# Performance work log

Hardware: AMD Instinct MI355X
Metric: run time of the kernel (lower is better)

The kernel has to match this reference:

```python
import jax, jax.numpy as jnp
import numpy as np

L = 4          # decoder layers (model_config "[4,[0],0]")
D = 1024       # d_model
H = 16         # n_head
DH = 64        # d_head
DI = 4096      # d_inner
V = 16000      # n_token (add_eot=False)
S = 1024       # seq len
B = 4          # batch
EPS = 1e-5


def _layer_norm(x, g, b):
    mu = jnp.mean(x, axis=-1, keepdims=True)
    var = jnp.mean(jnp.square(x - mu), axis=-1, keepdims=True)
    return (x - mu) * jax.lax.rsqrt(var + EPS) * g + b


def _rel_shift(x):
    # x: [b, n, q, k]
    b, n, q, k = x.shape
    zero_pad = jnp.zeros((b, n, q, 1), dtype=x.dtype)
    xp = jnp.concatenate([zero_pad, x], axis=3)        # [b,n,q,k+1]
    xp = xp.reshape(b, n, k + 1, q)
    return xp[:, :, 1:, :].reshape(b, n, q, k)


def setup_inputs() -> dict:
    key = jax.random.key(0)
    ks = list(jax.random.split(key, 24))
    sd = 0.02
    inp = {}
    inp["tokens"] = jax.random.randint(ks[0], (S, B), 0, V)
    inp["word_emb"] = jax.random.normal(ks[1], (V, D), jnp.float32) * sd
    inp["r_w_bias"] = jax.random.normal(ks[2], (H, DH), jnp.float32) * sd
    inp["r_r_bias"] = jax.random.normal(ks[3], (H, DH), jnp.float32) * sd
    inp["qkv_w"] = jax.random.normal(ks[4], (L, D, 3 * H * DH), jnp.float32) * sd
    inp["qkv_b"] = jnp.zeros((L, 3 * H * DH), jnp.float32)
    inp["r_kw"] = jax.random.normal(ks[5], (L, D, H * DH), jnp.float32) * sd
    inp["r_kb"] = jnp.zeros((L, H * DH), jnp.float32)
    inp["o_w"] = jax.random.normal(ks[6], (L, H * DH, D), jnp.float32) * sd
    inp["o_b"] = jnp.zeros((L, D), jnp.float32)
    inp["ln1_g"] = jnp.ones((L, D), jnp.float32)
    inp["ln1_b"] = jnp.zeros((L, D), jnp.float32)
    inp["ff1_w"] = jax.random.normal(ks[7], (L, D, DI), jnp.float32) * sd
    inp["ff1_b"] = jnp.zeros((L, DI), jnp.float32)
    inp["ff2_w"] = jax.random.normal(ks[8], (L, DI, D), jnp.float32) * sd
    inp["ff2_b"] = jnp.zeros((L, D), jnp.float32)
    inp["ln2_g"] = jnp.ones((L, D), jnp.float32)
    inp["ln2_b"] = jnp.zeros((L, D), jnp.float32)
    inp["final_w"] = jax.random.normal(ks[9], (D, V), jnp.float32) * sd
    inp["final_b"] = jnp.zeros((V,), jnp.float32)
    return inp


def reference(tokens, word_emb, r_w_bias, r_r_bias, qkv_w, qkv_b, r_kw, r_kb,
              o_w, o_b, ln1_g, ln1_b, ff1_w, ff1_b, ff2_w, ff2_b,
              ln2_g, ln2_b, final_w, final_b):
    s, b = tokens.shape
    h = word_emb[tokens]                                 # [S,B,D]
    # sinusoidal relative positions, pos_seq = klen-1 ... 0
    pos_seq = jnp.arange(s - 1, -1, -1, dtype=h.dtype)
    inv_freq = 1.0 / (10000.0 ** (jnp.arange(0, D, 2, dtype=h.dtype) / D))
    sinu = pos_seq[:, None] * inv_freq[None, :]
    r = jnp.concatenate([jnp.sin(sinu), jnp.cos(sinu)], axis=-1)   # [S,D]
    # causal mask: True = masked (j > i)
    mask = jnp.triu(jnp.ones((s, s), dtype=bool), k=1)
    scale = 1.0 / (DH ** 0.5)
    neg_inf = jnp.asarray(-jnp.inf, dtype=h.dtype)

    for l in range(L):
        qkv = h @ qkv_w[l] + qkv_b[l]                    # [S,B,3*H*DH]
        q, k, v = jnp.split(qkv, 3, axis=-1)
        q = q.reshape(s, b, H, DH)
        k = k.reshape(s, b, H, DH)
        v = v.reshape(s, b, H, DH)
        rk = (r @ r_kw[l] + r_kb[l]).reshape(s, H, DH)   # [S,H,DH]
        AC = jnp.einsum('ibnd,jbnd->bnij', q + r_w_bias, k)
        BD = jnp.einsum('ibnd,jnd->bnij', q + r_r_bias, rk)
        BD = _rel_shift(BD)
        score = scale * (AC + BD)
        score = jnp.where(mask[None, None, :, :], neg_inf, score)
        prob = jax.nn.softmax(score, axis=-1)
        vec = jnp.einsum('bnij,jbnd->ibnd', prob, v).reshape(s, b, H * DH)
        attn_out = vec @ o_w[l] + o_b[l]
        h = _layer_norm(h + attn_out, ln1_g[l], ln1_b[l])
        ff = jax.nn.gelu(h @ ff1_w[l] + ff1_b[l], approximate=False) @ ff2_w[l] + ff2_b[l]
        h = _layer_norm(h + ff, ln2_g[l], ln2_b[l])

    logits = h @ final_w + final_b                       # [S,B,V]
    return logits
```

## Files before the change

### kernel.cpp

```cpp
#include <hip/hip_runtime.h>

#define S 1024
#define Bb 4
#define Hh 16
#define DHh 64
#define Dm 1024
#define DIi 4096
#define Vv 16000
#define Lll 4

typedef __attribute__((ext_vector_type(4))) float f32x4;
typedef __attribute__((ext_vector_type(8))) __bf16 bf16x8;
typedef __attribute__((ext_vector_type(8))) unsigned short u16x8;
typedef __attribute__((ext_vector_type(4))) unsigned short u16x4;

__device__ __forceinline__ unsigned short f2bf(float f) {
  unsigned int u = __float_as_uint(f);
  u += 0x7fffu + ((u >> 16) & 1u);
  return (unsigned short)(u >> 16);
}
__device__ __forceinline__ float bf2f(unsigned short u) {
  return __uint_as_float(((unsigned int)u) << 16);
}

__device__ __forceinline__ void gload_lds16(const void* g, void* l) {
  __builtin_amdgcn_global_load_lds((const __attribute__((address_space(1))) unsigned int*)g,
                                   (__attribute__((address_space(3))) unsigned int*)l, 16, 0, 0);
}

__device__ __forceinline__ f32x4 mfma_bf16(bf16x8 a, bf16x8 b, f32x4 c) {
  return __builtin_amdgcn_mfma_f32_16x16x32_bf16(a, b, c, 0, 0, 0);
}

__global__ __launch_bounds__(256) void embed_k(const int* __restrict__ tokens,
                                               const float* __restrict__ we,
                                               float* __restrict__ h,
                                               unsigned short* __restrict__ hb) {
  int row = blockIdx.x;
  int t = threadIdx.x;
  int tok = tokens[row];
  f32x4 v = *(const f32x4*)&we[(long)tok * Dm + t * 4];
  *(f32x4*)&h[(long)row * Dm + t * 4] = v;
  u16x4 r;
#pragma unroll
  for (int e = 0; e < 4; ++e) r[e] = f2bf(v[e]);
  *(u16x4*)&hb[(long)row * Dm + t * 4] = r;
}

__global__ __launch_bounds__(256) void posr_k(unsigned short* __restrict__ r) {
  int idx = blockIdx.x * 256 + threadIdx.x;
  int u = idx >> 10, d = idx & 1023;
  float pos = (float)(S - 1 - u);
  int j = d & 511;
  float invf = powf(10000.0f, -(float)j * (1.0f / 512.0f));
  float a = pos * invf;
  r[idx] = f2bf(d < 512 ? sinf(a) : cosf(a));
}

__global__ __launch_bounds__(256) void wcvt_t(const float* __restrict__ W,
                                              unsigned short* __restrict__ WT,
                                              int Kd, int Nd) {
  __shared__ unsigned short tile[32][40];
  int n0 = blockIdx.x * 32, k0 = blockIdx.y * 32;
  const float* Wb = W + (long)blockIdx.z * Kd * Nd;
  unsigned short* WTb = WT + (long)blockIdx.z * Kd * Nd;
  int t = threadIdx.x;
  int rr = t >> 3, c4 = (t & 7) * 4;
  f32x4 v = *(const f32x4*)&Wb[(long)(k0 + rr) * Nd + n0 + c4];
#pragma unroll
  for (int e = 0; e < 4; ++e) tile[rr][c4 + e] = f2bf(v[e]);
  __syncthreads();
  if (t < 128) {
    int n = t >> 2, k8 = (t & 3) * 8;
    u16x8 pk;
#pragma unroll
    for (int e = 0; e < 8; ++e) pk[e] = tile[k8 + e][n];
    *(u16x8*)&WTb[(long)(n0 + n) * Kd + k0 + k8] = pk;
  }
}

template <int EPI>
__global__ __launch_bounds__(256) void gemm_bt(const unsigned short* __restrict__ A,
                                               const unsigned short* __restrict__ BT,
                                               const float* __restrict__ bias,
                                               void* __restrict__ Cout,
                                               int M, int N, int K, int ntn) {
  __shared__ unsigned short As[128 * 64];
  __shared__ unsigned short Bs[128 * 64];
  const int tid = threadIdx.x;
  const int lane = tid & 63;
  const int w = tid >> 6;
  const int nwg = gridDim.x;
  const int qq = nwg >> 3, rr = nwg & 7;
  const int xcd = blockIdx.x & 7, loc = blockIdx.x >> 3;
  const int wg = (xcd < rr ? xcd * (qq + 1) : rr * (qq + 1) + (xcd - rr) * qq) + loc;
  const int bn = (wg % ntn) * 128, bm = (wg / ntn) * 128;
  const int wr = (w >> 1) * 64, wc = (w & 1) * 64;
  const int la = lane & 15, lk = (lane >> 4) * 8;
  f32x4 acc[4][4] = {};

  const int rrow = tid >> 3;
  const int rcol = (tid & 7) * 8;
  const unsigned short* ag = A + (long)(bm + rrow) * K + rcol;
  const unsigned short* bg = BT + (long)(bn + rrow) * K + rcol;

  for (int k0 = 0; k0 < K; k0 += 64) {
    __syncthreads();
#pragma unroll
    for (int c = 0; c < 4; ++c) {
      gload_lds16(ag + (long)c * 32 * K + k0, &As[c * 2048 + w * 512]);
      gload_lds16(bg + (long)c * 32 * K + k0, &Bs[c * 2048 + w * 512]);
    }
    __syncthreads();
#pragma unroll
    for (int kk = 0; kk < 2; ++kk) {
      bf16x8 af[4], bq[4];
#pragma unroll
      for (int mi = 0; mi < 4; ++mi)
        af[mi] = *(const bf16x8*)&As[(wr + mi * 16 + la) * 64 + kk * 32 + lk];
#pragma unroll
      for (int ni = 0; ni < 4; ++ni)
        bq[ni] = *(const bf16x8*)&Bs[(wc + ni * 16 + la) * 64 + kk * 32 + lk];
#pragma unroll
      for (int mi = 0; mi < 4; ++mi)
#pragma unroll
        for (int ni = 0; ni < 4; ++ni)
          acc[mi][ni] = mfma_bf16(af[mi], bq[ni], acc[mi][ni]);
    }
  }
  const int cr = (lane >> 4) * 4;
#pragma unroll
  for (int mi = 0; mi < 4; ++mi) {
#pragma unroll
    for (int ni = 0; ni < 4; ++ni) {
      int col = bn + wc + ni * 16 + la;
      float bv = bias[col];
      int row = bm + wr + mi * 16 + cr;
#pragma unroll
      for (int e = 0; e < 4; ++e) {
        float v = acc[mi][ni][e] + bv;
        if (EPI == 0) {
          ((float*)Cout)[(long)(row + e) * N + col] = v;
        } else if (EPI == 1) {
          ((unsigned short*)Cout)[(long)(row + e) * N + col] = f2bf(v);
        } else {
          float g = 0.5f * v * (1.0f + erff(v * 0.70710678118f));
          ((unsigned short*)Cout)[(long)(row + e) * N + col] = f2bf(g);
        }
      }
    }
  }
}

__global__ __launch_bounds__(256) void qkv_prep(const unsigned short* __restrict__ q3,
                                                const float* __restrict__ rwb,
                                                const float* __restrict__ rrb,
                                                unsigned short* __restrict__ qw,
                                                unsigned short* __restrict__ qr,
                                                unsigned short* __restrict__ kb) {
  int idx = blockIdx.x * 256 + threadIdx.x;
  int c8 = (idx & 127) * 8;
  int row = idx >> 7;
  int s = row >> 2, b = row & 3;
  int n = c8 >> 6, d = c8 & 63;
  u16x8 qv = *(const u16x8*)&q3[(long)row * 3072 + c8];
  u16x8 kv = *(const u16x8*)&q3[(long)row * 3072 + 1024 + c8];
  long o = ((long)(b * Hh + n) * S + s) * 64 + d;
  u16x8 ow, orr;
#pragma unroll
  for (int e = 0; e < 8; ++e) {
    float q = bf2f(qv[e]);
    ow[e] = f2bf(q + rwb[c8 + e]);
    orr[e] = f2bf(q + rrb[c8 + e]);
  }
  *(u16x8*)&qw[o] = ow;
  *(u16x8*)&qr[o] = orr;
  *(u16x8*)&kb[o] = kv;
}

__global__ __launch_bounds__(256) void vt_prep(const unsigned short* __restrict__ q3,
                                               unsigned short* __restrict__ vT) {
  __shared__ unsigned short tile[64][72];
  const int it = blockIdx.x, bn = blockIdx.y;
  const int nh = bn & 15, bbv = bn >> 4;
  const int t = threadIdx.x;
  const int i0 = t >> 3, c8 = (t & 7) * 8;
#pragma unroll
  for (int c = 0; c < 2; ++c) {
    int i = i0 + c * 32;
    u16x8 v = *(const u16x8*)&q3[((long)(it * 64 + i) * Bb + bbv) * 3072 + 2048 + nh * 64 + c8];
    *(u16x8*)&tile[i][c8] = v;
  }
  __syncthreads();
  for (int cc = t; cc < 512; cc += 256) {
    int d = cc >> 3, i8 = (cc & 7) * 8;
    u16x8 pk;
#pragma unroll
    for (int e = 0; e < 8; ++e) pk[e] = tile[i8 + e][d];
    *(u16x8*)&vT[((long)bn * 64 + d) * S + it * 64 + i8] = pk;
  }
}

__global__ __launch_bounds__(256) void rkb_prep(const unsigned short* __restrict__ rkall,
                                                unsigned short* __restrict__ rkb) {
  int idx = blockIdx.x * 256 + threadIdx.x;
  int d8 = (idx & 7) * 8;
  int u = (idx >> 3) & 1023;
  int nl = idx >> 13;
  int l = nl >> 4, n = nl & 15;
  u16x8 v = *(const u16x8*)&rkall[(long)u * 4096 + l * 1024 + n * 64 + d8];
  *(u16x8*)&rkb[(long)idx * 8] = v;
}

__global__ __launch_bounds__(256) void attn_k(const unsigned short* __restrict__ qw,
                                              const unsigned short* __restrict__ qr,
                                              const unsigned short* __restrict__ kbuf,
                                              const unsigned short* __restrict__ vT,
                                              const unsigned short* __restrict__ rk,
                                              unsigned short* __restrict__ vec) {
  __shared__ unsigned short Ks[2][64 * 64];
  __shared__ unsigned short Vs[2][64 * 64];
  __shared__ unsigned short plds[4][16][72];
  const int tid = threadIdx.x, lane = tid & 63, w = tid >> 6;
  const int bn = blockIdx.x >> 3, pr = blockIdx.x & 7;
  const int nh = bn & 15, bbv = bn >> 4;
  const int la = lane & 15, hi = lane >> 4, lk = hi * 8;
  const int hi4 = hi * 4;
  const unsigned short* kbase = kbuf + (long)bn * S * 64;
  const unsigned short* vbase = vT + (long)bn * 64 * S;
  const unsigned short* rbase = rk + (long)nh * S * 64;

  const int q0 = w * 128 + lane;
  const int r0 = q0 >> 3, c0s = (q0 & 7) ^ (r0 & 7);
  const int q1 = q0 + 64;
  const int r1 = q1 >> 3, c1s = (q1 & 7) ^ (r1 & 7);

  int cur = 0;
#pragma unroll 1
  for (int half = 0; half < 2; ++half) {
    const int it = half ? (15 - pr) : pr;
    const int iw = it * 64 + w * 16;
    bf16x8 qwf[2], qrf[2];
    {
      const unsigned short* qp = qw + ((long)bn * S + iw + la) * 64 + lk;
      qwf[0] = *(const bf16x8*)qp;
      qwf[1] = *(const bf16x8*)(qp + 32);
      const unsigned short* qp2 = qr + ((long)bn * S + iw + la) * 64 + lk;
      qrf[0] = *(const bf16x8*)qp2;
      qrf[1] = *(const bf16x8*)(qp2 + 32);
    }
    f32x4 opv[4] = {};
    float m_[4] = {-3e38f, -3e38f, -3e38f, -3e38f};
    float l_[4] = {0.f, 0.f, 0.f, 0.f};

    gload_lds16(kbase + (long)r0 * 64 + c0s * 8, &Ks[cur][w * 1024]);
    gload_lds16(kbase + (long)r1 * 64 + c1s * 8, &Ks[cur][w * 1024 + 512]);
    gload_lds16(vbase + (long)r0 * S + c0s * 8, &Vs[cur][w * 1024]);
    gload_lds16(vbase + (long)r1 * S + c1s * 8, &Vs[cur][w * 1024 + 512]);
    __syncthreads();

    for (int jt = 0; jt <= it; ++jt) {
      const int j0 = jt * 64;
      const bool edge = (jt == it);
      if (jt < it) {
        const int jn = j0 + 64;
        gload_lds16(kbase + (long)(jn + r0) * 64 + c0s * 8, &Ks[cur ^ 1][w * 1024]);
        gload_lds16(kbase + (long)(jn + r1) * 64 + c1s * 8, &Ks[cur ^ 1][w * 1024 + 512]);
        gload_lds16(vbase + (long)r0 * S + jn + c0s * 8, &Vs[cur ^ 1][w * 1024]);
        gload_lds16(vbase + (long)r1 * S + jn + c1s * 8, &Vs[cur ^ 1][w * 1024 + 512]);
      }
      const int u0 = S - 16 - iw + j0;
      bf16x8 rf[10];
#pragma unroll
      for (int g = 0; g < 5; ++g) {
        int u = u0 + g * 16 + la;
        if (edge) u = (u > S - 1) ? (S - 1) : u;
        const unsigned short* rp = rbase + (long)u * 64 + lk;
        rf[2 * g] = *(const bf16x8*)rp;
        rf[2 * g + 1] = *(const bf16x8*)(rp + 32);
      }
      f32x4 ac[4] = {};
#pragma unroll
      for (int f = 0; f < 4; ++f) {
        int row = f * 16 + la;
        const unsigned short* kl = &Ks[cur][row * 64];
        bf16x8 k0 = *(const bf16x8*)(kl + (((hi) ^ (row & 7)) << 3));
        bf16x8 k1 = *(const bf16x8*)(kl + (((hi + 4) ^ (row & 7)) << 3));
        ac[f] = mfma_bf16(qwf[0], k0, ac[f]);
        ac[f] = mfma_bf16(qwf[1], k1, ac[f]);
      }
      f32x4 gg[5] = {};
#pragma unroll
      for (int g = 0; g < 5; ++g) {
        gg[g] = mfma_bf16(qrf[0], rf[2 * g], gg[g]);
        gg[g] = mfma_bf16(qrf[1], rf[2 * g + 1], gg[g]);
      }
      float p[4][4];
#pragma unroll
      for (int f = 0; f < 4; ++f) {
#pragma unroll
        for (int e = 0; e < 4; ++e) {
          int r = hi4 + e;
          float x = (la >= 15 - r) ? gg[f][e] : gg[f + 1][e];
          int src = (lane & 48) | ((la + 15 - r) & 15);
          float bd = __shfl(x, src, 64);
          float sc = (ac[f][e] + bd) * 0.125f;
          if (edge) {
            int i_ = iw + r, j_ = j0 + f * 16 + la;
            sc = (j_ > i_) ? -1e30f : sc;
          }
          p[f][e] = sc;
        }
      }
#pragma unroll
      for (int e = 0; e < 4; ++e) {
        float mx = fmaxf(fmaxf(p[0][e], p[1][e]), fmaxf(p[2][e], p[3][e]));
#pragma unroll
        for (int o = 1; o < 16; o <<= 1) mx = fmaxf(mx, __shfl_xor(mx, o, 64));
        float mnew = fmaxf(m_[e], mx);
        float alpha = __expf(m_[e] - mnew);
        m_[e] = mnew;
        float rs = 0.f;
#pragma unroll
        for (int f = 0; f < 4; ++f) {
          p[f][e] = __expf(p[f][e] - mnew);
          rs += p[f][e];
        }
        l_[e] = l_[e] * alpha + rs;
#pragma unroll
        for (int d = 0; d < 4; ++d) opv[d][e] *= alpha;
      }
#pragma unroll
      for (int f = 0; f < 4; ++f)
#pragma unroll
        for (int e = 0; e < 4; ++e)
          plds[w][hi4 + e][f * 16 + la] = f2bf(p[f][e]);
      bf16x8 pa0 = *(const bf16x8*)&plds[w][la][lk];
      bf16x8 pa1 = *(const bf16x8*)&plds[w][la][32 + lk];
#pragma unroll
      for (int d = 0; d < 4; ++d) {
        int dd = d * 16 + la;
        const unsigned short* vl = &Vs[cur][dd * 64];
        bf16x8 v0 = *(const bf16x8*)(vl + (((hi) ^ (dd & 7)) << 3));
        bf16x8 v1 = *(const bf16x8*)(vl + (((hi + 4) ^ (dd & 7)) << 3));
        opv[d] = mfma_bf16(pa0, v0, opv[d]);
        opv[d] = mfma_bf16(pa1, v1, opv[d]);
      }
      __syncthreads();
      if (jt < it) cur ^= 1;
    }
#pragma unroll
    for (int e = 0; e < 4; ++e) {
#pragma unroll
      for (int o = 1; o < 16; o <<= 1) l_[e] += __shfl_xor(l_[e], o, 64);
    }
#pragma unroll
    for (int d = 0; d < 4; ++d) {
#pragma unroll
      for (int e = 0; e < 4; ++e) {
        int i_ = iw + hi4 + e;
        int col = nh * 64 + d * 16 + la;
        vec[((long)i_ * Bb + bbv) * 1024 + col] = f2bf(opv[d][e] / l_[e]);
      }
    }
  }
}

__global__ __launch_bounds__(256) void add_ln(float* __restrict__ h, const float* __restrict__ x,
                                              const float* __restrict__ g, const float* __restrict__ b,
                                              unsigned short* __restrict__ hb) {
  __shared__ float red[8];
  int row = blockIdx.x, t = threadIdx.x;
  long base = (long)row * 1024 + t * 4;
  f32x4 hv = *(const f32x4*)&h[base];
  f32x4 xv = *(const f32x4*)&x[base];
  f32x4 y = hv + xv;
  float s = y[0] + y[1] + y[2] + y[3];
  float q = y[0] * y[0] + y[1] * y[1] + y[2] * y[2] + y[3] * y[3];
#pragma unroll
  for (int o = 1; o < 64; o <<= 1) {
    s += __shfl_xor(s, o, 64);
    q += __shfl_xor(q, o, 64);
  }
  int w = t >> 6, lane = t & 63;
  if (lane == 0) { red[w] = s; red[4 + w] = q; }
  __syncthreads();
  s = red[0] + red[1] + red[2] + red[3];
  q = red[4] + red[5] + red[6] + red[7];
  float mu = s * (1.0f / 1024.0f);
  float var = q * (1.0f / 1024.0f) - mu * mu;
  float rstd = rsqrtf(var + 1e-5f);
  f32x4 gv = *(const f32x4*)&g[t * 4];
  f32x4 bv = *(const f32x4*)&b[t * 4];
  f32x4 o;
  u16x4 ob;
#pragma unroll
  for (int e = 0; e < 4; ++e) {
    o[e] = (y[e] - mu) * rstd * gv[e] + bv[e];
    ob[e] = f2bf(o[e]);
  }
  *(f32x4*)&h[base] = o;
  *(u16x4*)&hb[base] = ob;
}

extern "C" void kernel_launch(void* const* d_in, const int* in_sizes, int n_in,
                              void* d_out, int out_size, void* d_ws, size_t ws_size,
                              hipStream_t stream) {
  const int* tokens = (const int*)d_in[0];
  const float* word_emb = (const float*)d_in[1];
  const float* rwb = (const float*)d_in[2];
  const float* rrb = (const float*)d_in[3];
  const float* qkv_w = (const float*)d_in[4];
  const float* qkv_b = (const float*)d_in[5];
  const float* r_kw = (const float*)d_in[6];
  const float* r_kb = (const float*)d_in[7];
  const float* o_w = (const float*)d_in[8];
  const float* o_b = (const float*)d_in[9];
  const float* ln1g = (const float*)d_in[10];
  const float* ln1b = (const float*)d_in[11];
  const float* ff1w = (const float*)d_in[12];
  const float* ff1b = (const float*)d_in[13];
  const float* ff2w = (const float*)d_in[14];
  const float* ff2b = (const float*)d_in[15];
  const float* ln2g = (const float*)d_in[16];
  const float* ln2b = (const float*)d_in[17];
  const float* fw = (const float*)d_in[18];
  const float* fb = (const float*)d_in[19];

  char* ws = (char*)d_ws;
  unsigned short* WBF = (unsigned short*)(ws);
  float* H = (float*)(ws + 33554432);
  unsigned short* HB = (unsigned short*)(ws + 50331648);
  unsigned short* GB = (unsigned short*)(ws + 58720256);
  unsigned short* RBF = (unsigned short*)(ws + 92274688);

  char* ob = (char*)d_out;
  float* OUTF = (float*)ob;
  unsigned short* OUTH = (unsigned short*)ob;
  unsigned short* QW = (unsigned short*)(ob + 67108864);
  unsigned short* QR = (unsigned short*)(ob + 75497472);
  unsigned short* KB = (unsigned short*)(ob + 83886080);
  unsigned short* VT = (unsigned short*)(ob + 92274688);
  unsigned short* RKB = (unsigned short*)(ob + 100663296);
  float* OUT = (float*)d_out;

  embed_k<<<4096, 256, 0, stream>>>(tokens, word_emb, H, HB);
  posr_k<<<4096, 256, 0, stream>>>(RBF);
  wcvt_t<<<dim3(32, 32, 4), 256, 0, stream>>>(r_kw, WBF, 1024, 1024);
  gemm_bt<1><<<256, 256, 0, stream>>>(RBF, WBF, r_kb, OUTH, 1024, 4096, 1024, 32);
  rkb_prep<<<2048, 256, 0, stream>>>(OUTH, RKB);

  for (int l = 0; l < Lll; ++l) {
    wcvt_t<<<dim3(96, 32, 1), 256, 0, stream>>>(qkv_w + (long)l * 1024 * 3072, WBF, 1024, 3072);
    gemm_bt<1><<<768, 256, 0, stream>>>(HB, WBF, qkv_b + l * 3072, OUTH, 4096, 3072, 1024, 24);
    qkv_prep<<<2048, 256, 0, stream>>>(OUTH, rwb, rrb, QW, QR, KB);
    vt_prep<<<dim3(16, 64), 256, 0, stream>>>(OUTH, VT);
    attn_k<<<512, 256, 0, stream>>>(QW, QR, KB, VT, RKB + (long)l * Hh * S * 64, HB);
    wcvt_t<<<dim3(32, 32, 1), 256, 0, stream>>>(o_w + (long)l * 1024 * 1024, WBF, 1024, 1024);
    gemm_bt<0><<<256, 256, 0, stream>>>(HB, WBF, o_b + l * 1024, OUTF, 4096, 1024, 1024, 8);
    add_ln<<<4096, 256, 0, stream>>>(H, OUTF, ln1g + l * 1024, ln1b + l * 1024, HB);

    wcvt_t<<<dim3(128, 32, 1), 256, 0, stream>>>(ff1w + (long)l * 1024 * 4096, WBF, 1024, 4096);
    gemm_bt<2><<<1024, 256, 0, stream>>>(HB, WBF, ff1b + l * 4096, GB, 4096, 4096, 1024, 32);
    wcvt_t<<<dim3(32, 128, 1), 256, 0, stream>>>(ff2w + (long)l * 4096 * 1024, WBF, 4096, 1024);
    gemm_bt<0><<<256, 256, 0, stream>>>(GB, WBF, ff2b + l * 1024, OUTF, 4096, 1024, 4096, 8);
    add_ln<<<4096, 256, 0, stream>>>(H, OUTF, ln2g + l * 1024, ln2b + l * 1024, HB);
  }

  wcvt_t<<<dim3(500, 32, 1), 256, 0, stream>>>(fw, WBF, 1024, 16000);
  gemm_bt<0><<<4000, 256, 0, stream>>>(HB, WBF, fb, OUT, 4096, 16000, 1024, 125);
}
```

Measured before the change: 1.700 ms.

## Replace 128x128 GEMM with 256x256 tiled, 4-stage pipelined GEMM kernel

Replaces the single-buffered 128x128 bf16 GEMM with a 512-thread 256x256 tile kernel. It uses a 4-deep LDS ring of K=32 slices loaded asynchronously, explicit vmcnt waits with one barrier per step, and raised priority around the MFMA block. The larger tile raises arithmetic intensity and the pipeline overlaps global loads with compute. The final projection pads N to 16128 with bounds checks, and weight conversion zero-fills out-of-range columns. The risks are small grids for the N=1024 GEMMs (only 64 workgroups, underfilling the GPU's many CUs) and higher register and LDS pressure.

```diff
diff --git a/kernel.cpp b/kernel.cpp
--- a/kernel.cpp
+++ b/kernel.cpp
@@ -62,11 +62,13 @@
                                               int Kd, int Nd) {
   __shared__ unsigned short tile[32][40];
   int n0 = blockIdx.x * 32, k0 = blockIdx.y * 32;
+  const bool inb = n0 < Nd;
   const float* Wb = W + (long)blockIdx.z * Kd * Nd;
   unsigned short* WTb = WT + (long)blockIdx.z * Kd * Nd;
   int t = threadIdx.x;
   int rr = t >> 3, c4 = (t & 7) * 4;
-  f32x4 v = *(const f32x4*)&Wb[(long)(k0 + rr) * Nd + n0 + c4];
+  f32x4 v = {0.f, 0.f, 0.f, 0.f};
+  if (inb) v = *(const f32x4*)&Wb[(long)(k0 + rr) * Nd + n0 + c4];
 #pragma unroll
   for (int e = 0; e < 4; ++e) tile[rr][c4 + e] = f2bf(v[e]);
   __syncthreads();
@@ -80,72 +82,99 @@
 }
 
 template <int EPI>
-__global__ __launch_bounds__(256) void gemm_bt(const unsigned short* __restrict__ A,
-                                               const unsigned short* __restrict__ BT,
-                                               const float* __restrict__ bias,
-                                               void* __restrict__ Cout,
-                                               int M, int N, int K, int ntn) {
-  __shared__ unsigned short As[128 * 64];
-  __shared__ unsigned short Bs[128 * 64];
-  const int tid = threadIdx.x;
-  const int lane = tid & 63;
-  const int w = tid >> 6;
+__global__ __launch_bounds__(512, 2) void gemm256(const unsigned short* __restrict__ A,
+                                                  const unsigned short* __restrict__ BT,
+                                                  const float* __restrict__ bias,
+                                                  void* __restrict__ Cout,
+                                                  int M, int N, int K,
+                                                  int ntm, int ntn, int morder) {
+  __shared__ unsigned short lds[65536];
+  unsigned short* Al = lds;
+  unsigned short* Bl = lds + 32768;
+  const int tid = threadIdx.x, lane = tid & 63, w = tid >> 6;
+  const int la = lane & 15, hi = lane >> 4;
   const int nwg = gridDim.x;
   const int qq = nwg >> 3, rr = nwg & 7;
   const int xcd = blockIdx.x & 7, loc = blockIdx.x >> 3;
   const int wg = (xcd < rr ? xcd * (qq + 1) : rr * (qq + 1) + (xcd - rr) * qq) + loc;
-  const int bn = (wg % ntn) * 128, bm = (wg / ntn) * 128;
-  const int wr = (w >> 1) * 64, wc = (w & 1) * 64;
-  const int la = lane & 15, lk = (lane >> 4) * 8;
-  f32x4 acc[4][4] = {};
-
-  const int rrow = tid >> 3;
-  const int rcol = (tid & 7) * 8;
-  const unsigned short* ag = A + (long)(bm + rrow) * K + rcol;
-  const unsigned short* bg = BT + (long)(bn + rrow) * K + rcol;
-
-  for (int k0 = 0; k0 < K; k0 += 64) {
-    __syncthreads();
-#pragma unroll
-    for (int c = 0; c < 4; ++c) {
-      gload_lds16(ag + (long)c * 32 * K + k0, &As[c * 2048 + w * 512]);
-      gload_lds16(bg + (long)c * 32 * K + k0, &Bs[c * 2048 + w * 512]);
-    }
-    __syncthreads();
-#pragma unroll
-    for (int kk = 0; kk < 2; ++kk) {
-      bf16x8 af[4], bq[4];
-#pragma unroll
-      for (int mi = 0; mi < 4; ++mi)
-        af[mi] = *(const bf16x8*)&As[(wr + mi * 16 + la) * 64 + kk * 32 + lk];
-#pragma unroll
-      for (int ni = 0; ni < 4; ++ni)
-        bq[ni] = *(const bf16x8*)&Bs[(wc + ni * 16 + la) * 64 + kk * 32 + lk];
-#pragma unroll
-      for (int mi = 0; mi < 4; ++mi)
-#pragma unroll
-        for (int ni = 0; ni < 4; ++ni)
-          acc[mi][ni] = mfma_bf16(af[mi], bq[ni], acc[mi][ni]);
-    }
-  }
-  const int cr = (lane >> 4) * 4;
-#pragma unroll
-  for (int mi = 0; mi < 4; ++mi) {
-#pragma unroll
-    for (int ni = 0; ni < 4; ++ni) {
-      int col = bn + wc + ni * 16 + la;
-      float bv = bias[col];
-      int row = bm + wr + mi * 16 + cr;
-#pragma unroll
-      for (int e = 0; e < 4; ++e) {
-        float v = acc[mi][ni][e] + bv;
-        if (EPI == 0) {
-          ((float*)Cout)[(long)(row + e) * N + col] = v;
-        } else if (EPI == 1) {
-          ((unsigned short*)Cout)[(long)(row + e) * N + col] = f2bf(v);
-        } else {
-          float g = 0.5f * v * (1.0f + erff(v * 0.70710678118f));
-          ((unsigned short*)Cout)[(long)(row + e) * N + col] = f2bf(g);
+  int bm, bn;
+  if (morder) { bm = (wg % ntm) * 256; bn = (wg / ntm) * 256; }
+  else        { bn = (wg % ntn) * 256; bm = (wg / ntn) * 256; }
+  const int wr = w >> 2, wc = w & 3;
+  f32x4 acc[8][4] = {};
+
+  const unsigned short* ag = A + (long)(bm + w * 16 + la) * K + hi * 8;
+  const unsigned short* bg = BT + (long)(bn + w * 16 + la) * K + hi * 8;
+  unsigned short* Asg = Al + w * 512;
+  unsigned short* Bsg = Bl + w * 512;
+  const unsigned short* Ard = Al + wr * 4096 + lane * 8;
+  const unsigned short* Brd = Bl + wc * 2048 + lane * 8;
+  const int NT = K >> 5;
+
+#define STAGE(t) { \
+    long ko_ = (long)(t) * 32; int bo_ = ((t) & 3) * 8192; \
+    gload_lds16(ag + ko_, Asg + bo_); \
+    gload_lds16(ag + ko_ + (long)128 * K, Asg + bo_ + 4096); \
+    gload_lds16(bg + ko_, Bsg + bo_); \
+    gload_lds16(bg + ko_ + (long)128 * K, Bsg + bo_ + 4096); }
+
+#define COMPUTE(t) { \
+    const int bo_ = ((t) & 3) * 8192; \
+    bf16x8 af[8], bq[4]; \
+    _Pragma("unroll") \
+    for (int m = 0; m < 8; ++m) af[m] = *(const bf16x8*)(Ard + bo_ + m * 512); \
+    _Pragma("unroll") \
+    for (int n = 0; n < 4; ++n) bq[n] = *(const bf16x8*)(Brd + bo_ + n * 512); \
+    __builtin_amdgcn_s_setprio(1); \
+    _Pragma("unroll") \
+    for (int m = 0; m < 8; ++m) \
+      _Pragma("unroll") \
+      for (int n = 0; n < 4; ++n) acc[m][n] = mfma_bf16(af[m], bq[n], acc[m][n]); \
+    __builtin_amdgcn_s_setprio(0); }
+
+  STAGE(0); STAGE(1); STAGE(2);
+  int t = 0;
+  for (; t < NT - 3; ++t) {
+    asm volatile("s_waitcnt vmcnt(8)" ::: "memory");
+    __builtin_amdgcn_s_barrier();
+    __builtin_amdgcn_sched_barrier(0);
+    STAGE(t + 3);
+    COMPUTE(t);
+  }
+  asm volatile("s_waitcnt vmcnt(8)" ::: "memory");
+  __builtin_amdgcn_s_barrier();
+  __builtin_amdgcn_sched_barrier(0);
+  COMPUTE(t); ++t;
+  asm volatile("s_waitcnt vmcnt(4)" ::: "memory");
+  __builtin_amdgcn_s_barrier();
+  __builtin_amdgcn_sched_barrier(0);
+  COMPUTE(t); ++t;
+  asm volatile("s_waitcnt vmcnt(0)" ::: "memory");
+  __builtin_amdgcn_s_barrier();
+  __builtin_amdgcn_sched_barrier(0);
+  COMPUTE(t);
+#undef STAGE
+#undef COMPUTE
+
+#pragma unroll
+  for (int m = 0; m < 8; ++m) {
+#pragma unroll
+    for (int n = 0; n < 4; ++n) {
+      int col = bn + wc * 64 + n * 16 + la;
+      if (col < N) {
+        float bv = bias[col];
+        int row = bm + wr * 128 + m * 16 + hi * 4;
+#pragma unroll
+        for (int e = 0; e < 4; ++e) {
+          float v = acc[m][n][e] + bv;
+          if (EPI == 0) {
+            ((float*)Cout)[(long)(row + e) * N + col] = v;
+          } else if (EPI == 1) {
+            ((unsigned short*)Cout)[(long)(row + e) * N + col] = f2bf(v);
+          } else {
+            float g = 0.5f * v * (1.0f + erff(v * 0.70710678118f));
+            ((unsigned short*)Cout)[(long)(row + e) * N + col] = f2bf(g);
+          }
         }
       }
     }
@@ -447,26 +476,26 @@
   embed_k<<<4096, 256, 0, stream>>>(tokens, word_emb, H, HB);
   posr_k<<<4096, 256, 0, stream>>>(RBF);
   wcvt_t<<<dim3(32, 32, 4), 256, 0, stream>>>(r_kw, WBF, 1024, 1024);
-  gemm_bt<1><<<256, 256, 0, stream>>>(RBF, WBF, r_kb, OUTH, 1024, 4096, 1024, 32);
+  gemm256<1><<<64, 512, 0, stream>>>(RBF, WBF, r_kb, OUTH, 1024, 4096, 1024, 4, 16, 0);
   rkb_prep<<<2048, 256, 0, stream>>>(OUTH, RKB);
 
   for (int l = 0; l < Lll; ++l) {
     wcvt_t<<<dim3(96, 32, 1), 256, 0, stream>>>(qkv_w + (long)l * 1024 * 3072, WBF, 1024, 3072);
-    gemm_bt<1><<<768, 256, 0, stream>>>(HB, WBF, qkv_b + l * 3072, OUTH, 4096, 3072, 1024, 24);
+    gemm256<1><<<192, 512, 0, stream>>>(HB, WBF, qkv_b + l * 3072, OUTH, 4096, 3072, 1024, 16, 12, 0);
     qkv_prep<<<2048, 256, 0, stream>>>(OUTH, rwb, rrb, QW, QR, KB);
     vt_prep<<<dim3(16, 64), 256, 0, stream>>>(OUTH, VT);
     attn_k<<<512, 256, 0, stream>>>(QW, QR, KB, VT, RKB + (long)l * Hh * S * 64, HB);
     wcvt_t<<<dim3(32, 32, 1), 256, 0, stream>>>(o_w + (long)l * 1024 * 1024, WBF, 1024, 1024);
-    gemm_bt<0><<<256, 256, 0, stream>>>(HB, WBF, o_b + l * 1024, OUTF, 4096, 1024, 1024, 8);
+    gemm256<0><<<64, 512, 0, stream>>>(HB, WBF, o_b + l * 1024, OUTF, 4096, 1024, 1024, 16, 4, 0);
     add_ln<<<4096, 256, 0, stream>>>(H, OUTF, ln1g + l * 1024, ln1b + l * 1024, HB);
 
     wcvt_t<<<dim3(128, 32, 1), 256, 0, stream>>>(ff1w + (long)l * 1024 * 4096, WBF, 1024, 4096);
-    gemm_bt<2><<<1024, 256, 0, stream>>>(HB, WBF, ff1b + l * 4096, GB, 4096, 4096, 1024, 32);
+    gemm256<2><<<256, 512, 0, stream>>>(HB, WBF, ff1b + l * 4096, GB, 4096, 4096, 1024, 16, 16, 0);
     wcvt_t<<<dim3(32, 128, 1), 256, 0, stream>>>(ff2w + (long)l * 4096 * 1024, WBF, 4096, 1024);
-    gemm_bt<0><<<256, 256, 0, stream>>>(GB, WBF, ff2b + l * 1024, OUTF, 4096, 1024, 4096, 8);
+    gemm256<0><<<64, 512, 0, stream>>>(GB, WBF, ff2b + l * 1024, OUTF, 4096, 1024, 4096, 16, 4, 0);
     add_ln<<<4096, 256, 0, stream>>>(H, OUTF, ln2g + l * 1024, ln2b + l * 1024, HB);
   }
 
-  wcvt_t<<<dim3(500, 32, 1), 256, 0, stream>>>(fw, WBF, 1024, 16000);
-  gemm_bt<0><<<4000, 256, 0, stream>>>(HB, WBF, fb, OUT, 4096, 16000, 1024, 125);
-}
+  wcvt_t<<<dim3(504, 32, 1), 256, 0, stream>>>(fw, WBF, 1024, 16000);
+  gemm256<0><<<1008, 512, 0, stream>>>(HB, WBF, fb, OUT, 4096, 16000, 1024, 16, 63, 1);
+}
```

Result: slower. 2.076 ms (+22.1%).

## Add 256x256 eight-wave GEMM kernel and lazy softmax rescaling in attention

Applied to the files above, without the earlier changes.

Adds a new 512-thread GEMM kernel with 256x256 output tiles, double-buffered direct-to-LDS loads, split fragment loads interleaved with MFMA phases and priority hints. It is used for the QKV, FF1 and final-logits projections. Padding the weight transpose to a multiple of 256 columns lets the last tile handle the ragged vocabulary. Separately, the attention online softmax now tracks one running max per row group and only rescales when the max grows by more than a threshold, which skips exp and multiply work. The lazy rescale risks overflow if values drift, and the larger tiles raise register and LDS pressure.

```diff
diff --git a/kernel.cpp b/kernel.cpp
--- a/kernel.cpp
+++ b/kernel.cpp
@@ -62,11 +62,13 @@
                                               int Kd, int Nd) {
   __shared__ unsigned short tile[32][40];
   int n0 = blockIdx.x * 32, k0 = blockIdx.y * 32;
+  const bool inb = n0 < Nd;
   const float* Wb = W + (long)blockIdx.z * Kd * Nd;
   unsigned short* WTb = WT + (long)blockIdx.z * Kd * Nd;
   int t = threadIdx.x;
   int rr = t >> 3, c4 = (t & 7) * 4;
-  f32x4 v = *(const f32x4*)&Wb[(long)(k0 + rr) * Nd + n0 + c4];
+  f32x4 v = {0.f, 0.f, 0.f, 0.f};
+  if (inb) v = *(const f32x4*)&Wb[(long)(k0 + rr) * Nd + n0 + c4];
 #pragma unroll
   for (int e = 0; e < 4; ++e) tile[rr][c4 + e] = f2bf(v[e]);
   __syncthreads();
@@ -76,6 +78,146 @@
 #pragma unroll
     for (int e = 0; e < 8; ++e) pk[e] = tile[k8 + e][n];
     *(u16x8*)&WTb[(long)(n0 + n) * Kd + k0 + k8] = pk;
+  }
+}
+
+template <int EPI>
+__global__ __launch_bounds__(512, 2) void gemm8(
+    const unsigned short* __restrict__ A, const unsigned short* __restrict__ BT,
+    const float* __restrict__ bias, void* __restrict__ Cout,
+    int M, int N, int K, int ntm, int ntn, int morder) {
+  __shared__ unsigned short lds[65536];
+  const int tid = threadIdx.x, lane = tid & 63, w = tid >> 6;
+  const int la = lane & 15, hi = lane >> 4;
+  const int nwg = gridDim.x;
+  const int qq = nwg >> 3, rr = nwg & 7;
+  const int xcd = blockIdx.x & 7, loc = blockIdx.x >> 3;
+  const int wg = (xcd < rr ? xcd * (qq + 1) : rr * (qq + 1) + (xcd - rr) * qq) + loc;
+  int bm, bn;
+  if (morder) { bm = (wg % ntm) * 256; bn = (wg / ntm) * 256; }
+  else        { bn = (wg % ntn) * 256; bm = (wg / ntn) * 256; }
+  const int wr = w >> 2, wc = w & 3;
+  f32x4 acc[8][4] = {};
+
+  const unsigned short* agS = A + (long)(bm + (w >> 1) * 16 + la) * K + ((w & 1) * 4 + hi) * 8;
+  const unsigned short* bgS = BT + (long)(bn + (w >> 1) * 16 + la) * K + ((w & 1) * 4 + hi) * 8;
+  const long cstep = (long)64 * K;
+  const int aoff = wr * 8192 + hi * 128 + la * 8;
+  const int boff = 32768 + wc * 4096 + hi * 128 + la * 8;
+  const int NT = K >> 6;
+  bf16x8 A0[4][2], A1[4][2], B0[2][2], B1[2][2];
+
+#define STAGE8(tt) { \
+    long ko_ = (long)(tt) * 64; int ab_ = ((tt) & 1) * 16384; \
+    _Pragma("unroll") \
+    for (int c = 0; c < 4; ++c) { \
+      gload_lds16(agS + ko_ + c * cstep, &lds[ab_ + c * 4096 + w * 512]); \
+      gload_lds16(bgS + ko_ + c * cstep, &lds[32768 + ab_ + c * 4096 + w * 512]); } }
+
+#define SYNC_LGKM  __builtin_amdgcn_s_barrier(); \
+    asm volatile("s_waitcnt lgkmcnt(0)" ::: "memory"); \
+    __builtin_amdgcn_sched_barrier(0)
+
+  STAGE8(0); STAGE8(1);
+  asm volatile("s_waitcnt vmcnt(8)" ::: "memory");
+  __builtin_amdgcn_s_barrier();
+
+#pragma unroll 1
+  for (int t = 0; t < NT; ++t) {
+    const int ab = (t & 1) * 16384;
+    const unsigned short* aRd = lds + ab + aoff;
+    const unsigned short* bRd = lds + ab + boff;
+#pragma unroll
+    for (int m = 0; m < 4; ++m)
+#pragma unroll
+      for (int kk = 0; kk < 2; ++kk) A0[m][kk] = *(const bf16x8*)(aRd + m * 1024 + kk * 512);
+#pragma unroll
+    for (int n = 0; n < 2; ++n)
+#pragma unroll
+      for (int kk = 0; kk < 2; ++kk) B0[n][kk] = *(const bf16x8*)(bRd + n * 1024 + kk * 512);
+    SYNC_LGKM;
+    __builtin_amdgcn_s_setprio(1);
+#pragma unroll
+    for (int m = 0; m < 4; ++m)
+#pragma unroll
+      for (int n = 0; n < 2; ++n) {
+        acc[m][n] = mfma_bf16(A0[m][0], B0[n][0], acc[m][n]);
+        acc[m][n] = mfma_bf16(A0[m][1], B0[n][1], acc[m][n]);
+      }
+    __builtin_amdgcn_s_setprio(0);
+    __builtin_amdgcn_s_barrier();
+#pragma unroll
+    for (int n = 0; n < 2; ++n)
+#pragma unroll
+      for (int kk = 0; kk < 2; ++kk) B1[n][kk] = *(const bf16x8*)(bRd + (2 + n) * 1024 + kk * 512);
+    SYNC_LGKM;
+    __builtin_amdgcn_s_setprio(1);
+#pragma unroll
+    for (int m = 0; m < 4; ++m)
+#pragma unroll
+      for (int n = 0; n < 2; ++n) {
+        acc[m][2 + n] = mfma_bf16(A0[m][0], B1[n][0], acc[m][2 + n]);
+        acc[m][2 + n] = mfma_bf16(A0[m][1], B1[n][1], acc[m][2 + n]);
+      }
+    __builtin_amdgcn_s_setprio(0);
+    __builtin_amdgcn_s_barrier();
+#pragma unroll
+    for (int m = 0; m < 4; ++m)
+#pragma unroll
+      for (int kk = 0; kk < 2; ++kk) A1[m][kk] = *(const bf16x8*)(aRd + (4 + m) * 1024 + kk * 512);
+    SYNC_LGKM;
+    __builtin_amdgcn_s_setprio(1);
+#pragma unroll
+    for (int m = 0; m < 4; ++m)
+#pragma unroll
+      for (int n = 0; n < 2; ++n) {
+        acc[4 + m][n] = mfma_bf16(A1[m][0], B0[n][0], acc[4 + m][n]);
+        acc[4 + m][n] = mfma_bf16(A1[m][1], B0[n][1], acc[4 + m][n]);
+      }
+    __builtin_amdgcn_s_setprio(0);
+    __builtin_amdgcn_s_barrier();
+    if (t + 2 < NT) { STAGE8(t + 2); }
+    __builtin_amdgcn_s_setprio(1);
+#pragma unroll
+    for (int m = 0; m < 4; ++m)
+#pragma unroll
+      for (int n = 0; n < 2; ++n) {
+        acc[4 + m][2 + n] = mfma_bf16(A1[m][0], B1[n][0], acc[4 + m][2 + n]);
+        acc[4 + m][2 + n] = mfma_bf16(A1[m][1], B1[n][1], acc[4 + m][2 + n]);
+      }
+    __builtin_amdgcn_s_setprio(0);
+    if (t + 2 < NT) {
+      asm volatile("s_waitcnt vmcnt(8)" ::: "memory");
+    } else if (t + 1 < NT) {
+      asm volatile("s_waitcnt vmcnt(0)" ::: "memory");
+    }
+    __builtin_amdgcn_s_barrier();
+  }
+#undef STAGE8
+#undef SYNC_LGKM
+
+#pragma unroll
+  for (int m = 0; m < 8; ++m) {
+#pragma unroll
+    for (int n = 0; n < 4; ++n) {
+      int col = bn + wc * 64 + n * 16 + la;
+      if (col < N) {
+        float bv = bias[col];
+        int row = bm + wr * 128 + m * 16 + hi * 4;
+#pragma unroll
+        for (int e = 0; e < 4; ++e) {
+          float v = acc[m][n][e] + bv;
+          if (EPI == 0) {
+            ((float*)Cout)[(long)(row + e) * N + col] = v;
+          } else if (EPI == 1) {
+            ((unsigned short*)Cout)[(long)(row + e) * N + col] = f2bf(v);
+          } else {
+            float g = 0.5f * v * (1.0f + erff(v * 0.70710678118f));
+            ((unsigned short*)Cout)[(long)(row + e) * N + col] = f2bf(g);
+          }
+        }
+      }
+    }
   }
 }
 
@@ -250,7 +392,7 @@
       qrf[1] = *(const bf16x8*)(qp2 + 32);
     }
     f32x4 opv[4] = {};
-    float m_[4] = {-3e38f, -3e38f, -3e38f, -3e38f};
+    float m_ = -3e38f;
     float l_[4] = {0.f, 0.f, 0.f, 0.f};
 
     gload_lds16(kbase + (long)r0 * 64 + c0s * 8, &Ks[cur][w * 1024]);
@@ -312,23 +454,33 @@
           p[f][e] = sc;
         }
       }
+      float mx = p[0][0];
+#pragma unroll
+      for (int f = 0; f < 4; ++f)
+#pragma unroll
+        for (int e = 0; e < 4; ++e) mx = fmaxf(mx, p[f][e]);
+#pragma unroll
+      for (int o = 1; o < 16; o <<= 1) mx = fmaxf(mx, __shfl_xor(mx, o, 64));
+      if (!__all(mx <= m_ + 8.0f)) {
+        float mnew = fmaxf(m_, mx);
+        float alpha = __expf(m_ - mnew);
+        m_ = mnew;
+#pragma unroll
+        for (int e = 0; e < 4; ++e) l_[e] *= alpha;
+#pragma unroll
+        for (int d = 0; d < 4; ++d)
+#pragma unroll
+          for (int e = 0; e < 4; ++e) opv[d][e] *= alpha;
+      }
 #pragma unroll
       for (int e = 0; e < 4; ++e) {
-        float mx = fmaxf(fmaxf(p[0][e], p[1][e]), fmaxf(p[2][e], p[3][e]));
-#pragma unroll
-        for (int o = 1; o < 16; o <<= 1) mx = fmaxf(mx, __shfl_xor(mx, o, 64));
-        float mnew = fmaxf(m_[e], mx);
-        float alpha = __expf(m_[e] - mnew);
-        m_[e] = mnew;
         float rs = 0.f;
 #pragma unroll
         for (int f = 0; f < 4; ++f) {
-          p[f][e] = __expf(p[f][e] - mnew);
+          p[f][e] = __expf(p[f][e] - m_);
           rs += p[f][e];
         }
-        l_[e] = l_[e] * alpha + rs;
-#pragma unroll
-        for (int d = 0; d < 4; ++d) opv[d][e] *= alpha;
+        l_[e] += rs;
       }
 #pragma unroll
       for (int f = 0; f < 4; ++f)
@@ -452,7 +604,7 @@
 
   for (int l = 0; l < Lll; ++l) {
     wcvt_t<<<dim3(96, 32, 1), 256, 0, stream>>>(qkv_w + (long)l * 1024 * 3072, WBF, 1024, 3072);
-    gemm_bt<1><<<768, 256, 0, stream>>>(HB, WBF, qkv_b + l * 3072, OUTH, 4096, 3072, 1024, 24);
+    gemm8<1><<<192, 512, 0, stream>>>(HB, WBF, qkv_b + l * 3072, OUTH, 4096, 3072, 1024, 16, 12, 1);
     qkv_prep<<<2048, 256, 0, stream>>>(OUTH, rwb, rrb, QW, QR, KB);
     vt_prep<<<dim3(16, 64), 256, 0, stream>>>(OUTH, VT);
     attn_k<<<512, 256, 0, stream>>>(QW, QR, KB, VT, RKB + (long)l * Hh * S * 64, HB);
@@ -461,12 +613,12 @@
     add_ln<<<4096, 256, 0, stream>>>(H, OUTF, ln1g + l * 1024, ln1b + l * 1024, HB);
 
     wcvt_t<<<dim3(128, 32, 1), 256, 0, stream>>>(ff1w + (long)l * 1024 * 4096, WBF, 1024, 4096);
-    gemm_bt<2><<<1024, 256, 0, stream>>>(HB, WBF, ff1b + l * 4096, GB, 4096, 4096, 1024, 32);
+    gemm8<2><<<256, 512, 0, stream>>>(HB, WBF, ff1b + l * 4096, GB, 4096, 4096, 1024, 16, 16, 1);
     wcvt_t<<<dim3(32, 128, 1), 256, 0, stream>>>(ff2w + (long)l * 4096 * 1024, WBF, 4096, 1024);
     gemm_bt<0><<<256, 256, 0, stream>>>(GB, WBF, ff2b + l * 1024, OUTF, 4096, 1024, 4096, 8);
     add_ln<<<4096, 256, 0, stream>>>(H, OUTF, ln2g + l * 1024, ln2b + l * 1024, HB);
   }
 
-  wcvt_t<<<dim3(500, 32, 1), 256, 0, stream>>>(fw, WBF, 1024, 16000);
-  gemm_bt<0><<<4000, 256, 0, stream>>>(HB, WBF, fb, OUT, 4096, 16000, 1024, 125);
-}
+  wcvt_t<<<dim3(504, 32, 1), 256, 0, stream>>>(fw, WBF, 1024, 16000);
+  gemm8<0><<<1008, 512, 0, stream>>>(HB, WBF, fb, OUT, 4096, 16000, 1024, 16, 63, 1);
+}
```

Result: slower. 1.859 ms (+9.3%).
